# Kernel optimization log

Measured on AMD Instinct MI355X. Metric: run time of the kernel, lower is better.

The kernel has to match this reference:

```python
import jax, jax.numpy as jnp
import numpy as np

B, N, E, C_IN, C_OUT = 16, 4096, 131072, 256, 256


def setup_inputs() -> dict:
    key = jax.random.key(0)
    k1, k2, k3, k4 = jax.random.split(key, 4)
    x = jax.random.normal(k1, (B, N, C_IN), dtype=jnp.float32)
    edge_index = jax.random.randint(k2, (B, 2, E), 0, N, dtype=jnp.int32)
    edge_weight = jax.random.uniform(k3, (B, E), dtype=jnp.float32)
    # glorot init for weight [C_in, C_out]
    scale = float(np.sqrt(6.0 / (C_IN + C_OUT)))
    W = jax.random.uniform(k4, (C_IN, C_OUT), dtype=jnp.float32, minval=-scale, maxval=scale)
    return {"x": x, "edge_index": edge_index, "edge_weight": edge_weight, "W": W}


def _gcn_one_graph(xi, ei, ewi, W):
    # xi: [N, C_in], ei: [2, E+N], ewi: [E+N]
    n = xi.shape[0]
    row, col = ei[0], ei[1]
    deg = jax.ops.segment_sum(ewi, row, num_segments=n)            # [N]
    deg_inv = jnp.where(deg > 0, jax.lax.rsqrt(deg), 0.0)          # deg^-0.5, inf -> 0
    norm = deg_inv[row] * ewi * deg_inv[col]                       # [E+N]
    xw = xi @ W                                                    # [N, C_out]
    msg = norm[:, None] * xw[col]                                  # gather + scale
    out = jax.ops.segment_sum(msg, row, num_segments=n)            # scatter-add to rows
    return jax.nn.relu(out)                                        # act = F.relu, bias=False


def reference(x, edge_index, edge_weight, W):
    b, n, _ = x.shape
    # add self loops with weight 1 (fill_value=1)
    loop = jnp.arange(n, dtype=edge_index.dtype)
    loop_idx = jnp.broadcast_to(jnp.stack([loop, loop])[None], (b, 2, n))
    ei = jnp.concatenate([edge_index, loop_idx], axis=-1)          # [B, 2, E+N]
    ew = jnp.concatenate([edge_weight, jnp.ones((b, n), x.dtype)], axis=-1)  # [B, E+N]
    return jax.vmap(_gcn_one_graph, in_axes=(0, 0, 0, None))(x, ei, ew, W)
```

## Files before the change

### kernel.cpp

```cpp
#include <hip/hip_runtime.h>
#include <cstdint>
#include <cstddef>

#define BB 16
#define NN 4096
#define EE 131072
#define CIN 256
#define COUT 256
#define NCH 16
#define CHE (EE / NCH)

typedef __attribute__((ext_vector_type(8))) _Float16 h16x8;
typedef __attribute__((ext_vector_type(4))) float f32x4;

#define GLDS16(g, l) __builtin_amdgcn_global_load_lds( \
    (const __attribute__((address_space(1))) uint32_t*)(g), \
    (__attribute__((address_space(3))) uint32_t*)(l), 16, 0, 0)

__global__ __launch_bounds__(256) void phaseA_kernel(const float* __restrict__ x, _Float16* __restrict__ xh,
                                                     const float* __restrict__ W, _Float16* __restrict__ wt,
                                                     const int* __restrict__ ei, const float* __restrict__ ew,
                                                     int* __restrict__ chist, float* __restrict__ wdeg) {
    __shared__ int h[NN];
    __shared__ float wh[NN];
    int bid = blockIdx.x;
    int tid = threadIdx.x;
    if (bid < BB * NCH) {
        int b = bid >> 4, c = bid & (NCH - 1);
        for (int i = tid; i < NN; i += 256) { h[i] = 0; wh[i] = 0.f; }
        __syncthreads();
        const int* rows = ei + (size_t)b * 2 * EE + (size_t)c * CHE;
        const float* w = ew + (size_t)b * EE + (size_t)c * CHE;
        #pragma unroll 4
        for (int j = 0; j < CHE / 256; ++j) {
            int row = rows[j * 256 + tid];
            float wv = w[j * 256 + tid];
            atomicAdd(&h[row], 1);
            atomicAdd(&wh[row], wv);
        }
        __syncthreads();
        int* co = chist + ((size_t)b * NCH + c) * NN;
        float* wo = wdeg + ((size_t)b * NCH + c) * NN;
        for (int i = tid; i < NN; i += 256) { co[i] = h[i]; wo[i] = wh[i]; }
    } else if (bid < BB * NCH + (BB * NN * CIN) / (256 * 8)) {
        size_t u = (size_t)(bid - BB * NCH) * 256 + tid;
        const float* g = &x[u * 8];
        float4 f0 = *reinterpret_cast<const float4*>(g);
        float4 f1 = *reinterpret_cast<const float4*>(g + 4);
        h16x8 v;
        v[0] = (_Float16)f0.x; v[1] = (_Float16)f0.y; v[2] = (_Float16)f0.z; v[3] = (_Float16)f0.w;
        v[4] = (_Float16)f1.x; v[5] = (_Float16)f1.y; v[6] = (_Float16)f1.z; v[7] = (_Float16)f1.w;
        *reinterpret_cast<h16x8*>(&xh[u * 8]) = v;
    } else {
        int n = bid - (BB * NCH + (BB * NN * CIN) / (256 * 8));
        int k = tid;
        wt[n * CIN + k] = (_Float16)W[(size_t)k * COUT + n];
    }
}

__global__ __launch_bounds__(1024) void scanfused_kernel(const int* __restrict__ chist, const float* __restrict__ wdeg,
                                                         int* __restrict__ chunkbase, int* __restrict__ roff,
                                                         float* __restrict__ dinv) {
    int b = blockIdx.x, tid = threadIdx.x;
    int wid = tid >> 6, lane = tid & 63;
    __shared__ int wsum[16];
    __shared__ int wbase[16];
    __shared__ int gtot_s;
    int carry = 0;
    for (int g = 0; g < 4; ++g) {
        int r = g * 1024 + tid;
        int cv[NCH];
        int tot = 0;
        float dsum = 1.0f;
        #pragma unroll
        for (int c = 0; c < NCH; ++c) {
            size_t idx = ((size_t)b * NCH + c) * NN + r;
            cv[c] = chist[idx];
            tot += cv[c];
            dsum += wdeg[idx];
        }
        dinv[b * NN + r] = rsqrtf(dsum);
        int incl = tot;
        #pragma unroll
        for (int off = 1; off < 64; off <<= 1) {
            int t = __shfl_up(incl, off, 64);
            if (lane >= off) incl += t;
        }
        if (lane == 63) wsum[wid] = incl;
        __syncthreads();
        if (wid == 0) {
            int v = (lane < 16) ? wsum[lane] : 0;
            int winc = v;
            #pragma unroll
            for (int off = 1; off < 16; off <<= 1) {
                int t = __shfl_up(winc, off, 64);
                if (lane >= off) winc += t;
            }
            if (lane < 16) wbase[lane] = winc - v;
            if (lane == 15) gtot_s = winc;
        }
        __syncthreads();
        int excl = carry + wbase[wid] + (incl - tot);
        roff[b * NN + r] = excl;
        int acc = excl;
        #pragma unroll
        for (int c = 0; c < NCH; ++c) {
            chunkbase[((size_t)b * NCH + c) * NN + r] = acc;
            acc += cv[c];
        }
        carry += gtot_s;
        __syncthreads();
    }
}

__global__ __launch_bounds__(256) void gemm_glds_kernel(const _Float16* __restrict__ xh, const _Float16* __restrict__ wt,
                                                        _Float16* __restrict__ xw) {
    __shared__ _Float16 As[128 * 64];
    __shared__ _Float16 Bs[128 * 64];
    int tid = threadIdx.x;
    int lane = tid & 63;
    int wave = tid >> 6;
    int bx = blockIdx.x >> 1, by = blockIdx.x & 1;
    int row0 = bx * 128, col0 = by * 128;
    int wr = wave >> 1, wc = wave & 1;
    int hi = lane >> 4, lo = lane & 15;
    int lr = lane >> 3, lk = (lane & 7) * 8;
    f32x4 acc[4][4] = {};

    for (int kk = 0; kk < CIN; kk += 64) {
        #pragma unroll
        for (int j = 0; j < 4; ++j) {
            int seg = j * 4 + wave;
            const _Float16* ga = &xh[(size_t)(row0 + seg * 8 + lr) * CIN + kk + lk];
            const _Float16* gb = &wt [(size_t)(col0 + seg * 8 + lr) * CIN + kk + lk];
            GLDS16(ga, &As[seg * 512]);
            GLDS16(gb, &Bs[seg * 512]);
        }
        __syncthreads();
        #pragma unroll
        for (int ks = 0; ks < 2; ++ks) {
            h16x8 a[4], b[4];
            #pragma unroll
            for (int m = 0; m < 4; ++m)
                a[m] = *reinterpret_cast<const h16x8*>(&As[(wr * 64 + m * 16 + lo) * 64 + ks * 32 + 8 * hi]);
            #pragma unroll
            for (int n = 0; n < 4; ++n)
                b[n] = *reinterpret_cast<const h16x8*>(&Bs[(wc * 64 + n * 16 + lo) * 64 + ks * 32 + 8 * hi]);
            #pragma unroll
            for (int m = 0; m < 4; ++m)
                #pragma unroll
                for (int n = 0; n < 4; ++n)
                    acc[m][n] = __builtin_amdgcn_mfma_f32_16x16x32_f16(a[m], b[n], acc[m][n], 0, 0, 0);
        }
        __syncthreads();
    }
    #pragma unroll
    for (int m = 0; m < 4; ++m)
        #pragma unroll
        for (int n = 0; n < 4; ++n)
            #pragma unroll
            for (int r = 0; r < 4; ++r) {
                int row = row0 + wr * 64 + m * 16 + hi * 4 + r;
                int col = col0 + wc * 64 + n * 16 + lo;
                xw[(size_t)row * COUT + col] = (_Float16)acc[m][n][r];
            }
}

__global__ __launch_bounds__(256) void scatter2_kernel(const int* __restrict__ ei, const float* __restrict__ ew,
                                                       const float* __restrict__ dinv, const int* __restrict__ chunkbase,
                                                       int2* __restrict__ csr) {
    __shared__ int basebuf[NN];
    __shared__ float dinvs[NN];
    int bid = blockIdx.x;
    int xcd = bid & 7;
    int j = bid >> 3;
    int b = xcd * 2 + (j >> 4);
    int c = j & (NCH - 1);
    int tid = threadIdx.x;
    for (int i = tid; i < NN; i += 256) {
        basebuf[i] = chunkbase[((size_t)b * NCH + c) * NN + i];
        dinvs[i] = dinv[b * NN + i];
    }
    __syncthreads();
    const int* rows = ei + (size_t)b * 2 * EE + (size_t)c * CHE;
    const int* cols = rows + EE;
    const float* w = ew + (size_t)b * EE + (size_t)c * CHE;
    int2* cs = csr + (size_t)b * EE;
    #pragma unroll 4
    for (int jj = 0; jj < CHE / 256; ++jj) {
        int e = jj * 256 + tid;
        int row = rows[e];
        int col = cols[e];
        float nm = dinvs[row] * w[e] * dinvs[col];
        int pos = atomicAdd(&basebuf[row], 1);
        int2 pk; pk.x = col * (COUT * 2); pk.y = __float_as_int(nm);
        cs[pos] = pk;
    }
}

#define ACCH(nm, r) { \
    a0 += (nm) * (float)(r)[0]; a1 += (nm) * (float)(r)[1]; \
    a2 += (nm) * (float)(r)[2]; a3 += (nm) * (float)(r)[3]; \
    a4 += (nm) * (float)(r)[4]; a5 += (nm) * (float)(r)[5]; \
    a6 += (nm) * (float)(r)[6]; a7 += (nm) * (float)(r)[7]; }

__global__ __launch_bounds__(256) void aggregate_kernel(const _Float16* __restrict__ xw, const float* __restrict__ dinv,
                                                        const int* __restrict__ roff, const int2* __restrict__ csr,
                                                        float* __restrict__ out) {
    int bid = blockIdx.x;
    int xcd = bid & 7;
    int idx = bid >> 3;
    int b = xcd * 2 + (idx >> 10);
    int rowblk = idx & 1023;
    int wave = threadIdx.x >> 6;
    int lane = threadIdx.x & 63;
    int n = rowblk * 4 + wave;
    bool hiHalf = lane >= 32;
    int sub = lane & 31;
    int lanebyte = sub * 16;

    const int* rb = roff + b * NN;
    int s = __builtin_amdgcn_readfirstlane(rb[n]);
    int eRaw = (n == NN - 1) ? EE : rb[n + 1];
    int e = __builtin_amdgcn_readfirstlane(eRaw);
    int cnt = e - s;
    const int2* cs = csr + (size_t)b * EE + s;

    const char* xwbase = (const char*)(xw + (size_t)b * NN * COUT);
    float a0 = 0.f, a1 = 0.f, a2 = 0.f, a3 = 0.f, a4 = 0.f, a5 = 0.f, a6 = 0.f, a7 = 0.f;

    {
        float di = dinv[b * NN + n];
        float sn = hiHalf ? 0.f : di * di;
        h16x8 r = *reinterpret_cast<const h16x8*>(xwbase + (size_t)n * (COUT * 2) + lanebyte);
        ACCH(sn, r);
    }

    int m = cnt & ~7;
    int i = 0;
    for (; i < m; i += 8) {
        int2 q[8];
        #pragma unroll
        for (int u = 0; u < 8; ++u) q[u] = cs[i + u];
        #pragma unroll
        for (int u = 0; u < 4; ++u) {
            int offx = (hiHalf ? q[2 * u + 1].x : q[2 * u].x) + lanebyte;
            float nm = __int_as_float(hiHalf ? q[2 * u + 1].y : q[2 * u].y);
            h16x8 r = *reinterpret_cast<const h16x8*>(xwbase + (uint32_t)offx);
            ACCH(nm, r);
        }
    }
    if (i < cnt) {
        #pragma unroll
        for (int u = 0; u < 4; ++u) {
            int j0 = i + 2 * u, j1 = j0 + 1;
            int jc0 = (j0 < cnt) ? j0 : cnt - 1;
            int jc1 = (j1 < cnt) ? j1 : cnt - 1;
            int2 q0 = cs[jc0];
            int2 q1 = cs[jc1];
            int offx = (hiHalf ? q1.x : q0.x) + lanebyte;
            float nm0 = (j0 < cnt) ? __int_as_float(q0.y) : 0.f;
            float nm1 = (j1 < cnt) ? __int_as_float(q1.y) : 0.f;
            float nm = hiHalf ? nm1 : nm0;
            h16x8 r = *reinterpret_cast<const h16x8*>(xwbase + (uint32_t)offx);
            ACCH(nm, r);
        }
    }

    a0 += __shfl(a0, lane ^ 32, 64); a1 += __shfl(a1, lane ^ 32, 64);
    a2 += __shfl(a2, lane ^ 32, 64); a3 += __shfl(a3, lane ^ 32, 64);
    a4 += __shfl(a4, lane ^ 32, 64); a5 += __shfl(a5, lane ^ 32, 64);
    a6 += __shfl(a6, lane ^ 32, 64); a7 += __shfl(a7, lane ^ 32, 64);

    float4 o = hiHalf
        ? make_float4(fmaxf(a4, 0.f), fmaxf(a5, 0.f), fmaxf(a6, 0.f), fmaxf(a7, 0.f))
        : make_float4(fmaxf(a0, 0.f), fmaxf(a1, 0.f), fmaxf(a2, 0.f), fmaxf(a3, 0.f));
    float* orow = out + ((size_t)b * NN + n) * COUT + sub * 8 + (hiHalf ? 4 : 0);
    *reinterpret_cast<float4*>(orow) = o;
}

__global__ __launch_bounds__(256) void cvt_wt_kernel(const float* __restrict__ W, _Float16* __restrict__ wt) {
    int n = blockIdx.x;
    int k = threadIdx.x;
    wt[n * CIN + k] = (_Float16)W[(size_t)k * COUT + n];
}

__global__ __launch_bounds__(256) void init_deg_kernel(float* __restrict__ deg, float v) {
    int i = blockIdx.x * 256 + threadIdx.x;
    if (i < BB * NN) deg[i] = v;
}

__global__ __launch_bounds__(256) void deg_only_kernel(const int* __restrict__ ei, const float* __restrict__ ew,
                                                       float* __restrict__ deg) {
    int idx = blockIdx.x * 256 + threadIdx.x;
    if (idx >= BB * EE) return;
    int b = idx / EE, e = idx - b * EE;
    atomicAdd(&deg[b * NN + ei[(size_t)b * 2 * EE + e]], ew[(size_t)b * EE + e]);
}

__global__ __launch_bounds__(256) void deginv_kernel(const float* __restrict__ deg, float* __restrict__ dinv) {
    int i = blockIdx.x * 256 + threadIdx.x;
    if (i < BB * NN) {
        float d = deg[i];
        dinv[i] = (d > 0.0f) ? rsqrtf(d) : 0.0f;
    }
}

__global__ __launch_bounds__(256) void gemm_f32src_kernel(const float* __restrict__ x, const _Float16* __restrict__ wt,
                                                          _Float16* __restrict__ xw) {
    __shared__ _Float16 As[128][64];
    __shared__ _Float16 Bs[128][64];
    int tid = threadIdx.x;
    int lane = tid & 63;
    int wave = tid >> 6;
    int row0 = blockIdx.x * 128;
    int col0 = blockIdx.y * 128;
    int wr = wave >> 1, wc = wave & 1;
    int hi = lane >> 4, lo = lane & 15;
    f32x4 acc[4][4] = {};
    for (int kk = 0; kk < CIN; kk += 64) {
        #pragma unroll
        for (int j = 0; j < 4; ++j) {
            int c = j * 256 + tid;
            int r = c >> 3, kq = c & 7;
            const float* g = &x[(size_t)(row0 + r) * CIN + kk + 8 * kq];
            float4 f0 = *reinterpret_cast<const float4*>(g);
            float4 f1 = *reinterpret_cast<const float4*>(g + 4);
            h16x8 v;
            v[0] = (_Float16)f0.x; v[1] = (_Float16)f0.y; v[2] = (_Float16)f0.z; v[3] = (_Float16)f0.w;
            v[4] = (_Float16)f1.x; v[5] = (_Float16)f1.y; v[6] = (_Float16)f1.z; v[7] = (_Float16)f1.w;
            *reinterpret_cast<h16x8*>(&As[r][8 * kq]) = v;
        }
        #pragma unroll
        for (int j = 0; j < 4; ++j) {
            int c = j * 256 + tid;
            int r = c >> 3, kq = c & 7;
            *reinterpret_cast<h16x8*>(&Bs[r][8 * kq]) =
                *reinterpret_cast<const h16x8*>(&wt[(size_t)(col0 + r) * CIN + kk + 8 * kq]);
        }
        __syncthreads();
        #pragma unroll
        for (int ks = 0; ks < 2; ++ks) {
            h16x8 a[4], b[4];
            #pragma unroll
            for (int m = 0; m < 4; ++m)
                a[m] = *reinterpret_cast<const h16x8*>(&As[wr * 64 + m * 16 + lo][ks * 32 + 8 * hi]);
            #pragma unroll
            for (int n = 0; n < 4; ++n)
                b[n] = *reinterpret_cast<const h16x8*>(&Bs[wc * 64 + n * 16 + lo][ks * 32 + 8 * hi]);
            #pragma unroll
            for (int m = 0; m < 4; ++m)
                #pragma unroll
                for (int n = 0; n < 4; ++n)
                    acc[m][n] = __builtin_amdgcn_mfma_f32_16x16x32_f16(a[m], b[n], acc[m][n], 0, 0, 0);
        }
        __syncthreads();
    }
    #pragma unroll
    for (int m = 0; m < 4; ++m)
        #pragma unroll
        for (int n = 0; n < 4; ++n)
            #pragma unroll
            for (int r = 0; r < 4; ++r) {
                int row = row0 + wr * 64 + m * 16 + hi * 4 + r;
                int col = col0 + wc * 64 + n * 16 + lo;
                xw[(size_t)row * COUT + col] = (_Float16)acc[m][n][r];
            }
}

__global__ __launch_bounds__(256) void self_kernel(const _Float16* __restrict__ xw, const float* __restrict__ dinv,
                                                   float* __restrict__ out) {
    int bn = blockIdx.x;
    int c = threadIdx.x;
    float di = dinv[bn];
    out[(size_t)bn * COUT + c] = di * di * (float)xw[(size_t)bn * COUT + c];
}

__global__ __launch_bounds__(256) void scatter_atomic_kernel(const int* __restrict__ ei, const float* __restrict__ ew,
                                                             const float* __restrict__ dinv,
                                                             const _Float16* __restrict__ xw, float* __restrict__ out) {
    int be = blockIdx.x;
    int b = be / EE, e = be - b * EE;
    int c = threadIdx.x;
    int row = ei[(size_t)b * 2 * EE + e];
    int col = ei[(size_t)b * 2 * EE + EE + e];
    float w = ew[(size_t)b * EE + e];
    float nm = dinv[b * NN + row] * w * dinv[b * NN + col];
    const _Float16* xwb = xw + (size_t)b * NN * COUT;
    atomicAdd(&out[((size_t)b * NN + row) * COUT + c], nm * (float)xwb[(size_t)col * COUT + c]);
}

__global__ __launch_bounds__(256) void relu_kernel(float* __restrict__ out) {
    size_t i = (size_t)blockIdx.x * 256 + threadIdx.x;
    out[i] = fmaxf(out[i], 0.0f);
}

extern "C" void kernel_launch(void* const* d_in, const int* in_sizes, int n_in,
                              void* d_out, int out_size, void* d_ws, size_t ws_size,
                              hipStream_t stream) {
    const float* x  = (const float*)d_in[0];
    const int*   ei = (const int*)d_in[1];
    const float* ew = (const float*)d_in[2];
    const float* Wm = (const float*)d_in[3];
    float* out = (float*)d_out;

    char* ws = (char*)d_ws;
    size_t off = 0;
    auto alloc = [&](size_t bytes) -> void* {
        void* p = ws + off;
        off += (bytes + 255) & ~(size_t)255;
        return p;
    };
    _Float16* xw        = (_Float16*)alloc((size_t)BB * NN * COUT * 2);
    _Float16* xh        = (_Float16*)alloc((size_t)BB * NN * CIN * 2);
    int*      chist     = (int*)alloc((size_t)BB * NCH * NN * 4);
    float*    wdeg      = (float*)alloc((size_t)BB * NCH * NN * 4);
    int*      chunkbase = (int*)alloc((size_t)BB * NCH * NN * 4);
    int*      roff      = (int*)alloc((size_t)BB * NN * 4);
    float*    dinv      = (float*)alloc((size_t)BB * NN * 4);
    _Float16* wt        = (_Float16*)alloc((size_t)CIN * COUT * 2);
    int2*     csr       = (int2*)xh;
    float*    deg_fb    = (float*)chist;
    bool use_csr = (ws_size >= off);

    if (use_csr) {
        const int xcvtBlocks = (BB * NN * CIN) / (256 * 8);
        phaseA_kernel<<<BB * NCH + xcvtBlocks + COUT, 256, 0, stream>>>(x, xh, Wm, wt, ei, ew, chist, wdeg);
        scanfused_kernel<<<BB, 1024, 0, stream>>>(chist, wdeg, chunkbase, roff, dinv);
        gemm_glds_kernel<<<(BB * NN / 128) * (COUT / 128), 256, 0, stream>>>(xh, wt, xw);
        scatter2_kernel<<<BB * NCH, 256, 0, stream>>>(ei, ew, dinv, chunkbase, csr);
        aggregate_kernel<<<BB * NN / 4, 256, 0, stream>>>(xw, dinv, roff, csr, out);
    } else {
        const int bnBlocks = (BB * NN) / 256;
        cvt_wt_kernel<<<COUT, CIN, 0, stream>>>(Wm, wt);
        init_deg_kernel<<<bnBlocks, 256, 0, stream>>>(deg_fb, 1.0f);
        deg_only_kernel<<<(BB * EE) / 256, 256, 0, stream>>>(ei, ew, deg_fb);
        deginv_kernel<<<bnBlocks, 256, 0, stream>>>(deg_fb, dinv);
        dim3 ggrid((BB * NN) / 128, COUT / 128);
        gemm_f32src_kernel<<<ggrid, 256, 0, stream>>>(x, wt, xw);
        self_kernel<<<BB * NN, 256, 0, stream>>>(xw, dinv, out);
        scatter_atomic_kernel<<<BB * EE, 256, 0, stream>>>(ei, ew, dinv, xw, out);
        relu_kernel<<<(BB * NN * COUT) / 256, 256, 0, stream>>>(out);
    }
}
```

Before: 135.6 us.

## Fuse fp32-to-fp16 conversion of x into a full-width GEMM and use fma_mix aggregation

Drops the separate pass that converted x to fp16 in phaseA, so the GEMM now loads fp32 x directly and converts it while staging into LDS. Each GEMM block now covers all 256 output columns (128x256 tile, 8 column fragments per wave), so x is read once rather than once per column half. The aggregation inner loop replaces the half-to-float conversions plus multiply-adds with inline v_fma_mix_f32 on packed halves. The CSR buffer gets its own workspace allocation instead of aliasing xh. The trade-offs are losing the async global_load_lds staging, more accumulator registers per wave and therefore lower occupancy, and a grid half as large.

```diff
diff --git a/kernel.cpp b/kernel.cpp
--- a/kernel.cpp
+++ b/kernel.cpp
@@ -13,12 +13,7 @@
 typedef __attribute__((ext_vector_type(8))) _Float16 h16x8;
 typedef __attribute__((ext_vector_type(4))) float f32x4;
 
-#define GLDS16(g, l) __builtin_amdgcn_global_load_lds( \
-    (const __attribute__((address_space(1))) uint32_t*)(g), \
-    (__attribute__((address_space(3))) uint32_t*)(l), 16, 0, 0)
-
-__global__ __launch_bounds__(256) void phaseA_kernel(const float* __restrict__ x, _Float16* __restrict__ xh,
-                                                     const float* __restrict__ W, _Float16* __restrict__ wt,
+__global__ __launch_bounds__(256) void phaseA_kernel(const float* __restrict__ W, _Float16* __restrict__ wt,
                                                      const int* __restrict__ ei, const float* __restrict__ ew,
                                                      int* __restrict__ chist, float* __restrict__ wdeg) {
     __shared__ int h[NN];
@@ -42,17 +37,8 @@
         int* co = chist + ((size_t)b * NCH + c) * NN;
         float* wo = wdeg + ((size_t)b * NCH + c) * NN;
         for (int i = tid; i < NN; i += 256) { co[i] = h[i]; wo[i] = wh[i]; }
-    } else if (bid < BB * NCH + (BB * NN * CIN) / (256 * 8)) {
-        size_t u = (size_t)(bid - BB * NCH) * 256 + tid;
-        const float* g = &x[u * 8];
-        float4 f0 = *reinterpret_cast<const float4*>(g);
-        float4 f1 = *reinterpret_cast<const float4*>(g + 4);
-        h16x8 v;
-        v[0] = (_Float16)f0.x; v[1] = (_Float16)f0.y; v[2] = (_Float16)f0.z; v[3] = (_Float16)f0.w;
-        v[4] = (_Float16)f1.x; v[5] = (_Float16)f1.y; v[6] = (_Float16)f1.z; v[7] = (_Float16)f1.w;
-        *reinterpret_cast<h16x8*>(&xh[u * 8]) = v;
     } else {
-        int n = bid - (BB * NCH + (BB * NN * CIN) / (256 * 8));
+        int n = bid - BB * NCH;
         int k = tid;
         wt[n * CIN + k] = (_Float16)W[(size_t)k * COUT + n];
     }
@@ -113,43 +99,52 @@
     }
 }
 
-__global__ __launch_bounds__(256) void gemm_glds_kernel(const _Float16* __restrict__ xh, const _Float16* __restrict__ wt,
-                                                        _Float16* __restrict__ xw) {
+__global__ __launch_bounds__(256) void gemm_f32wide_kernel(const float* __restrict__ x, const _Float16* __restrict__ wt,
+                                                           _Float16* __restrict__ xw) {
     __shared__ _Float16 As[128 * 64];
-    __shared__ _Float16 Bs[128 * 64];
+    __shared__ _Float16 Bs[256 * 64];
     int tid = threadIdx.x;
     int lane = tid & 63;
     int wave = tid >> 6;
-    int bx = blockIdx.x >> 1, by = blockIdx.x & 1;
-    int row0 = bx * 128, col0 = by * 128;
+    int row0 = blockIdx.x * 128;
     int wr = wave >> 1, wc = wave & 1;
     int hi = lane >> 4, lo = lane & 15;
-    int lr = lane >> 3, lk = (lane & 7) * 8;
-    f32x4 acc[4][4] = {};
+    f32x4 acc[4][8] = {};
 
     for (int kk = 0; kk < CIN; kk += 64) {
         #pragma unroll
         for (int j = 0; j < 4; ++j) {
-            int seg = j * 4 + wave;
-            const _Float16* ga = &xh[(size_t)(row0 + seg * 8 + lr) * CIN + kk + lk];
-            const _Float16* gb = &wt [(size_t)(col0 + seg * 8 + lr) * CIN + kk + lk];
-            GLDS16(ga, &As[seg * 512]);
-            GLDS16(gb, &Bs[seg * 512]);
+            int c = j * 256 + tid;
+            int r = c >> 3, kq = c & 7;
+            const float* g = &x[(size_t)(row0 + r) * CIN + kk + 8 * kq];
+            float4 f0 = *reinterpret_cast<const float4*>(g);
+            float4 f1 = *reinterpret_cast<const float4*>(g + 4);
+            h16x8 v;
+            v[0] = (_Float16)f0.x; v[1] = (_Float16)f0.y; v[2] = (_Float16)f0.z; v[3] = (_Float16)f0.w;
+            v[4] = (_Float16)f1.x; v[5] = (_Float16)f1.y; v[6] = (_Float16)f1.z; v[7] = (_Float16)f1.w;
+            *reinterpret_cast<h16x8*>(&As[r * 64 + 8 * kq]) = v;
+        }
+        #pragma unroll
+        for (int j = 0; j < 8; ++j) {
+            int c = j * 256 + tid;
+            int r = c >> 3, kq = c & 7;
+            *reinterpret_cast<h16x8*>(&Bs[r * 64 + 8 * kq]) =
+                *reinterpret_cast<const h16x8*>(&wt[(size_t)r * CIN + kk + 8 * kq]);
         }
         __syncthreads();
         #pragma unroll
         for (int ks = 0; ks < 2; ++ks) {
-            h16x8 a[4], b[4];
+            h16x8 a[4], b[8];
             #pragma unroll
             for (int m = 0; m < 4; ++m)
                 a[m] = *reinterpret_cast<const h16x8*>(&As[(wr * 64 + m * 16 + lo) * 64 + ks * 32 + 8 * hi]);
             #pragma unroll
-            for (int n = 0; n < 4; ++n)
-                b[n] = *reinterpret_cast<const h16x8*>(&Bs[(wc * 64 + n * 16 + lo) * 64 + ks * 32 + 8 * hi]);
+            for (int n = 0; n < 8; ++n)
+                b[n] = *reinterpret_cast<const h16x8*>(&Bs[(wc * 128 + n * 16 + lo) * 64 + ks * 32 + 8 * hi]);
             #pragma unroll
             for (int m = 0; m < 4; ++m)
                 #pragma unroll
-                for (int n = 0; n < 4; ++n)
+                for (int n = 0; n < 8; ++n)
                     acc[m][n] = __builtin_amdgcn_mfma_f32_16x16x32_f16(a[m], b[n], acc[m][n], 0, 0, 0);
         }
         __syncthreads();
@@ -157,11 +152,11 @@
     #pragma unroll
     for (int m = 0; m < 4; ++m)
         #pragma unroll
-        for (int n = 0; n < 4; ++n)
+        for (int n = 0; n < 8; ++n)
             #pragma unroll
             for (int r = 0; r < 4; ++r) {
                 int row = row0 + wr * 64 + m * 16 + hi * 4 + r;
-                int col = col0 + wc * 64 + n * 16 + lo;
+                int col = wc * 128 + n * 16 + lo;
                 xw[(size_t)row * COUT + col] = (_Float16)acc[m][n][r];
             }
 }
@@ -198,11 +193,15 @@
     }
 }
 
-#define ACCH(nm, r) { \
-    a0 += (nm) * (float)(r)[0]; a1 += (nm) * (float)(r)[1]; \
-    a2 += (nm) * (float)(r)[2]; a3 += (nm) * (float)(r)[3]; \
-    a4 += (nm) * (float)(r)[4]; a5 += (nm) * (float)(r)[5]; \
-    a6 += (nm) * (float)(r)[6]; a7 += (nm) * (float)(r)[7]; }
+#define MIXLO(acc_, w_, nm_) asm("v_fma_mix_f32 %0, %1, %2, %0 op_sel:[0,0,0] op_sel_hi:[1,0,0]" \
+                                 : "+v"(acc_) : "v"(w_), "v"(nm_));
+#define MIXHI(acc_, w_, nm_) asm("v_fma_mix_f32 %0, %1, %2, %0 op_sel:[1,0,0] op_sel_hi:[1,0,0]" \
+                                 : "+v"(acc_) : "v"(w_), "v"(nm_));
+#define ACCMIX(w_, nm_) { \
+    MIXLO(a0, (w_).x, nm_); MIXHI(a1, (w_).x, nm_); \
+    MIXLO(a2, (w_).y, nm_); MIXHI(a3, (w_).y, nm_); \
+    MIXLO(a4, (w_).z, nm_); MIXHI(a5, (w_).z, nm_); \
+    MIXLO(a6, (w_).w, nm_); MIXHI(a7, (w_).w, nm_); }
 
 __global__ __launch_bounds__(256) void aggregate_kernel(const _Float16* __restrict__ xw, const float* __restrict__ dinv,
                                                         const int* __restrict__ roff, const int2* __restrict__ csr,
@@ -232,8 +231,8 @@
     {
         float di = dinv[b * NN + n];
         float sn = hiHalf ? 0.f : di * di;
-        h16x8 r = *reinterpret_cast<const h16x8*>(xwbase + (size_t)n * (COUT * 2) + lanebyte);
-        ACCH(sn, r);
+        uint4 w = *reinterpret_cast<const uint4*>(xwbase + (size_t)n * (COUT * 2) + lanebyte);
+        ACCMIX(w, sn);
     }
 
     int m = cnt & ~7;
@@ -246,8 +245,8 @@
         for (int u = 0; u < 4; ++u) {
             int offx = (hiHalf ? q[2 * u + 1].x : q[2 * u].x) + lanebyte;
             float nm = __int_as_float(hiHalf ? q[2 * u + 1].y : q[2 * u].y);
-            h16x8 r = *reinterpret_cast<const h16x8*>(xwbase + (uint32_t)offx);
-            ACCH(nm, r);
+            uint4 w = *reinterpret_cast<const uint4*>(xwbase + (uint32_t)offx);
+            ACCMIX(w, nm);
         }
     }
     if (i < cnt) {
@@ -262,8 +261,8 @@
             float nm0 = (j0 < cnt) ? __int_as_float(q0.y) : 0.f;
             float nm1 = (j1 < cnt) ? __int_as_float(q1.y) : 0.f;
             float nm = hiHalf ? nm1 : nm0;
-            h16x8 r = *reinterpret_cast<const h16x8*>(xwbase + (uint32_t)offx);
-            ACCH(nm, r);
+            uint4 w = *reinterpret_cast<const uint4*>(xwbase + (uint32_t)offx);
+            ACCMIX(w, nm);
         }
     }
 
@@ -412,22 +411,20 @@
         return p;
     };
     _Float16* xw        = (_Float16*)alloc((size_t)BB * NN * COUT * 2);
-    _Float16* xh        = (_Float16*)alloc((size_t)BB * NN * CIN * 2);
+    int2*     csr       = (int2*)alloc((size_t)BB * EE * 8);
     int*      chist     = (int*)alloc((size_t)BB * NCH * NN * 4);
     float*    wdeg      = (float*)alloc((size_t)BB * NCH * NN * 4);
     int*      chunkbase = (int*)alloc((size_t)BB * NCH * NN * 4);
     int*      roff      = (int*)alloc((size_t)BB * NN * 4);
     float*    dinv      = (float*)alloc((size_t)BB * NN * 4);
     _Float16* wt        = (_Float16*)alloc((size_t)CIN * COUT * 2);
-    int2*     csr       = (int2*)xh;
     float*    deg_fb    = (float*)chist;
     bool use_csr = (ws_size >= off);
 
     if (use_csr) {
-        const int xcvtBlocks = (BB * NN * CIN) / (256 * 8);
-        phaseA_kernel<<<BB * NCH + xcvtBlocks + COUT, 256, 0, stream>>>(x, xh, Wm, wt, ei, ew, chist, wdeg);
+        phaseA_kernel<<<BB * NCH + COUT, 256, 0, stream>>>(Wm, wt, ei, ew, chist, wdeg);
         scanfused_kernel<<<BB, 1024, 0, stream>>>(chist, wdeg, chunkbase, roff, dinv);
-        gemm_glds_kernel<<<(BB * NN / 128) * (COUT / 128), 256, 0, stream>>>(xh, wt, xw);
+        gemm_f32wide_kernel<<<BB * NN / 128, 256, 0, stream>>>(x, wt, xw);
         scatter2_kernel<<<BB * NCH, 256, 0, stream>>>(ei, ew, dinv, chunkbase, csr);
         aggregate_kernel<<<BB * NN / 4, 256, 0, stream>>>(xw, dinv, roff, csr, out);
     } else {
```

Result: slower. 139.9 us (+3.2%).

## Fuse CSR scatter into GEMM launch and pack CSR entries to 32 bits

Applied to the files above, without the earlier changes.

Runs the CSR scatter blocks and the fp16 GEMM tiles in a single launch so the two independent stages overlap. CSR entries are packed into one 32-bit word holding a 16-bit column and an fp16 norm, halving CSR traffic. The aggregate kernel decodes them with v_fma_mix_f32 inline asm, avoiding separate half-to-float conversions. The fp16 norm reduces precision, and the CSR buffer now reuses the degree-histogram workspace.

```diff
diff --git a/kernel.cpp b/kernel.cpp
--- a/kernel.cpp
+++ b/kernel.cpp
@@ -113,99 +113,106 @@
     }
 }
 
-__global__ __launch_bounds__(256) void gemm_glds_kernel(const _Float16* __restrict__ xh, const _Float16* __restrict__ wt,
-                                                        _Float16* __restrict__ xw) {
-    __shared__ _Float16 As[128 * 64];
-    __shared__ _Float16 Bs[128 * 64];
+__global__ __launch_bounds__(256) void gemm_scatter_kernel(const _Float16* __restrict__ xh, const _Float16* __restrict__ wt,
+                                                           _Float16* __restrict__ xw,
+                                                           const int* __restrict__ ei, const float* __restrict__ ew,
+                                                           const float* __restrict__ dinv, const int* __restrict__ chunkbase,
+                                                           uint32_t* __restrict__ csr) {
+    __shared__ __align__(16) char smem[32768];
+    int bid = blockIdx.x;
     int tid = threadIdx.x;
-    int lane = tid & 63;
-    int wave = tid >> 6;
-    int bx = blockIdx.x >> 1, by = blockIdx.x & 1;
-    int row0 = bx * 128, col0 = by * 128;
-    int wr = wave >> 1, wc = wave & 1;
-    int hi = lane >> 4, lo = lane & 15;
-    int lr = lane >> 3, lk = (lane & 7) * 8;
-    f32x4 acc[4][4] = {};
-
-    for (int kk = 0; kk < CIN; kk += 64) {
-        #pragma unroll
-        for (int j = 0; j < 4; ++j) {
-            int seg = j * 4 + wave;
-            const _Float16* ga = &xh[(size_t)(row0 + seg * 8 + lr) * CIN + kk + lk];
-            const _Float16* gb = &wt [(size_t)(col0 + seg * 8 + lr) * CIN + kk + lk];
-            GLDS16(ga, &As[seg * 512]);
-            GLDS16(gb, &Bs[seg * 512]);
-        }
-        __syncthreads();
-        #pragma unroll
-        for (int ks = 0; ks < 2; ++ks) {
-            h16x8 a[4], b[4];
-            #pragma unroll
-            for (int m = 0; m < 4; ++m)
-                a[m] = *reinterpret_cast<const h16x8*>(&As[(wr * 64 + m * 16 + lo) * 64 + ks * 32 + 8 * hi]);
-            #pragma unroll
-            for (int n = 0; n < 4; ++n)
-                b[n] = *reinterpret_cast<const h16x8*>(&Bs[(wc * 64 + n * 16 + lo) * 64 + ks * 32 + 8 * hi]);
-            #pragma unroll
-            for (int m = 0; m < 4; ++m)
+    if (bid < 256) {
+        int* basebuf = (int*)smem;
+        float* dinvs = (float*)(smem + 16384);
+        int b = bid >> 4, c = bid & (NCH - 1);
+        for (int i = tid; i < NN; i += 256) {
+            basebuf[i] = chunkbase[((size_t)b * NCH + c) * NN + i];
+            dinvs[i] = dinv[b * NN + i];
+        }
+        __syncthreads();
+        const int* rows = ei + (size_t)b * 2 * EE + (size_t)c * CHE;
+        const int* cols = rows + EE;
+        const float* w = ew + (size_t)b * EE + (size_t)c * CHE;
+        uint32_t* cs = csr + (size_t)b * EE;
+        #pragma unroll 4
+        for (int jj = 0; jj < CHE / 256; ++jj) {
+            int e = jj * 256 + tid;
+            int row = rows[e];
+            int col = cols[e];
+            float nm = dinvs[row] * w[e] * dinvs[col];
+            int pos = atomicAdd(&basebuf[row], 1);
+            uint32_t nmh = (uint32_t)__builtin_bit_cast(unsigned short, (_Float16)nm);
+            cs[pos] = ((uint32_t)col << 16) | nmh;
+        }
+    } else {
+        _Float16* As = (_Float16*)smem;
+        _Float16* Bs = As + 128 * 64;
+        int g = bid - 256;
+        int lane = tid & 63;
+        int wave = tid >> 6;
+        int bx = g >> 1, by = g & 1;
+        int row0 = bx * 128, col0 = by * 128;
+        int wr = wave >> 1, wc = wave & 1;
+        int hi = lane >> 4, lo = lane & 15;
+        int lr = lane >> 3, lk = (lane & 7) * 8;
+        f32x4 acc[4][4] = {};
+
+        for (int kk = 0; kk < CIN; kk += 64) {
+            #pragma unroll
+            for (int j = 0; j < 4; ++j) {
+                int seg = j * 4 + wave;
+                const _Float16* ga = &xh[(size_t)(row0 + seg * 8 + lr) * CIN + kk + lk];
+                const _Float16* gb = &wt [(size_t)(col0 + seg * 8 + lr) * CIN + kk + lk];
+                GLDS16(ga, &As[seg * 512]);
+                GLDS16(gb, &Bs[seg * 512]);
+            }
+            __syncthreads();
+            #pragma unroll
+            for (int ks = 0; ks < 2; ++ks) {
+                h16x8 a[4], b[4];
+                #pragma unroll
+                for (int m = 0; m < 4; ++m)
+                    a[m] = *reinterpret_cast<const h16x8*>(&As[(wr * 64 + m * 16 + lo) * 64 + ks * 32 + 8 * hi]);
                 #pragma unroll
                 for (int n = 0; n < 4; ++n)
-                    acc[m][n] = __builtin_amdgcn_mfma_f32_16x16x32_f16(a[m], b[n], acc[m][n], 0, 0, 0);
-        }
-        __syncthreads();
-    }
-    #pragma unroll
-    for (int m = 0; m < 4; ++m)
-        #pragma unroll
-        for (int n = 0; n < 4; ++n)
-            #pragma unroll
-            for (int r = 0; r < 4; ++r) {
-                int row = row0 + wr * 64 + m * 16 + hi * 4 + r;
-                int col = col0 + wc * 64 + n * 16 + lo;
-                xw[(size_t)row * COUT + col] = (_Float16)acc[m][n][r];
+                    b[n] = *reinterpret_cast<const h16x8*>(&Bs[(wc * 64 + n * 16 + lo) * 64 + ks * 32 + 8 * hi]);
+                #pragma unroll
+                for (int m = 0; m < 4; ++m)
+                    #pragma unroll
+                    for (int n = 0; n < 4; ++n)
+                        acc[m][n] = __builtin_amdgcn_mfma_f32_16x16x32_f16(a[m], b[n], acc[m][n], 0, 0, 0);
             }
-}
-
-__global__ __launch_bounds__(256) void scatter2_kernel(const int* __restrict__ ei, const float* __restrict__ ew,
-                                                       const float* __restrict__ dinv, const int* __restrict__ chunkbase,
-                                                       int2* __restrict__ csr) {
-    __shared__ int basebuf[NN];
-    __shared__ float dinvs[NN];
-    int bid = blockIdx.x;
-    int xcd = bid & 7;
-    int j = bid >> 3;
-    int b = xcd * 2 + (j >> 4);
-    int c = j & (NCH - 1);
-    int tid = threadIdx.x;
-    for (int i = tid; i < NN; i += 256) {
-        basebuf[i] = chunkbase[((size_t)b * NCH + c) * NN + i];
-        dinvs[i] = dinv[b * NN + i];
-    }
-    __syncthreads();
-    const int* rows = ei + (size_t)b * 2 * EE + (size_t)c * CHE;
-    const int* cols = rows + EE;
-    const float* w = ew + (size_t)b * EE + (size_t)c * CHE;
-    int2* cs = csr + (size_t)b * EE;
-    #pragma unroll 4
-    for (int jj = 0; jj < CHE / 256; ++jj) {
-        int e = jj * 256 + tid;
-        int row = rows[e];
-        int col = cols[e];
-        float nm = dinvs[row] * w[e] * dinvs[col];
-        int pos = atomicAdd(&basebuf[row], 1);
-        int2 pk; pk.x = col * (COUT * 2); pk.y = __float_as_int(nm);
-        cs[pos] = pk;
-    }
-}
-
-#define ACCH(nm, r) { \
-    a0 += (nm) * (float)(r)[0]; a1 += (nm) * (float)(r)[1]; \
-    a2 += (nm) * (float)(r)[2]; a3 += (nm) * (float)(r)[3]; \
-    a4 += (nm) * (float)(r)[4]; a5 += (nm) * (float)(r)[5]; \
-    a6 += (nm) * (float)(r)[6]; a7 += (nm) * (float)(r)[7]; }
+            __syncthreads();
+        }
+        #pragma unroll
+        for (int m = 0; m < 4; ++m)
+            #pragma unroll
+            for (int n = 0; n < 4; ++n)
+                #pragma unroll
+                for (int r = 0; r < 4; ++r) {
+                    int row = row0 + wr * 64 + m * 16 + hi * 4 + r;
+                    int col = col0 + wc * 64 + n * 16 + lo;
+                    xw[(size_t)row * COUT + col] = (_Float16)acc[m][n][r];
+                }
+    }
+}
+
+#define MIXQLO(acc_, w_, qv_) asm("v_fma_mix_f32 %0, %1, %2, %0 op_sel:[0,0,0] op_sel_hi:[1,1,0]" \
+                                  : "+v"(acc_) : "v"(w_), "v"(qv_));
+#define MIXQHI(acc_, w_, qv_) asm("v_fma_mix_f32 %0, %1, %2, %0 op_sel:[1,0,0] op_sel_hi:[1,1,0]" \
+                                  : "+v"(acc_) : "v"(w_), "v"(qv_));
+#define ACCMIXQ(w_, qv_) { \
+    MIXQLO(a0, (w_).x, qv_); MIXQHI(a1, (w_).x, qv_); \
+    MIXQLO(a2, (w_).y, qv_); MIXQHI(a3, (w_).y, qv_); \
+    MIXQLO(a4, (w_).z, qv_); MIXQHI(a5, (w_).z, qv_); \
+    MIXQLO(a6, (w_).w, qv_); MIXQHI(a7, (w_).w, qv_); }
+#define MIXSLO(acc_, w_, nm_) asm("v_fma_mix_f32 %0, %1, %2, %0 op_sel:[0,0,0] op_sel_hi:[1,0,0]" \
+                                  : "+v"(acc_) : "v"(w_), "v"(nm_));
+#define MIXSHI(acc_, w_, nm_) asm("v_fma_mix_f32 %0, %1, %2, %0 op_sel:[1,0,0] op_sel_hi:[1,0,0]" \
+                                  : "+v"(acc_) : "v"(w_), "v"(nm_));
 
 __global__ __launch_bounds__(256) void aggregate_kernel(const _Float16* __restrict__ xw, const float* __restrict__ dinv,
-                                                        const int* __restrict__ roff, const int2* __restrict__ csr,
+                                                        const int* __restrict__ roff, const uint32_t* __restrict__ csr,
                                                         float* __restrict__ out) {
     int bid = blockIdx.x;
     int xcd = bid & 7;
@@ -217,14 +224,14 @@
     int n = rowblk * 4 + wave;
     bool hiHalf = lane >= 32;
     int sub = lane & 31;
-    int lanebyte = sub * 16;
+    uint32_t lanebyte = sub * 16;
 
     const int* rb = roff + b * NN;
     int s = __builtin_amdgcn_readfirstlane(rb[n]);
     int eRaw = (n == NN - 1) ? EE : rb[n + 1];
     int e = __builtin_amdgcn_readfirstlane(eRaw);
     int cnt = e - s;
-    const int2* cs = csr + (size_t)b * EE + s;
+    const uint32_t* cs = csr + (size_t)b * EE + s;
 
     const char* xwbase = (const char*)(xw + (size_t)b * NN * COUT);
     float a0 = 0.f, a1 = 0.f, a2 = 0.f, a3 = 0.f, a4 = 0.f, a5 = 0.f, a6 = 0.f, a7 = 0.f;
@@ -232,38 +239,39 @@
     {
         float di = dinv[b * NN + n];
         float sn = hiHalf ? 0.f : di * di;
-        h16x8 r = *reinterpret_cast<const h16x8*>(xwbase + (size_t)n * (COUT * 2) + lanebyte);
-        ACCH(sn, r);
+        uint4 w = *reinterpret_cast<const uint4*>(xwbase + (size_t)n * (COUT * 2) + lanebyte);
+        MIXSLO(a0, w.x, sn); MIXSHI(a1, w.x, sn);
+        MIXSLO(a2, w.y, sn); MIXSHI(a3, w.y, sn);
+        MIXSLO(a4, w.z, sn); MIXSHI(a5, w.z, sn);
+        MIXSLO(a6, w.w, sn); MIXSHI(a7, w.w, sn);
     }
 
     int m = cnt & ~7;
     int i = 0;
     for (; i < m; i += 8) {
-        int2 q[8];
+        uint32_t q[8];
         #pragma unroll
         for (int u = 0; u < 8; ++u) q[u] = cs[i + u];
         #pragma unroll
         for (int u = 0; u < 4; ++u) {
-            int offx = (hiHalf ? q[2 * u + 1].x : q[2 * u].x) + lanebyte;
-            float nm = __int_as_float(hiHalf ? q[2 * u + 1].y : q[2 * u].y);
-            h16x8 r = *reinterpret_cast<const h16x8*>(xwbase + (uint32_t)offx);
-            ACCH(nm, r);
+            uint32_t qv = hiHalf ? q[2 * u + 1] : q[2 * u];
+            uint32_t offx = ((qv >> 16) << 9) + lanebyte;
+            uint4 w = *reinterpret_cast<const uint4*>(xwbase + offx);
+            ACCMIXQ(w, qv);
         }
     }
     if (i < cnt) {
         #pragma unroll
         for (int u = 0; u < 4; ++u) {
             int j0 = i + 2 * u, j1 = j0 + 1;
-            int jc0 = (j0 < cnt) ? j0 : cnt - 1;
-            int jc1 = (j1 < cnt) ? j1 : cnt - 1;
-            int2 q0 = cs[jc0];
-            int2 q1 = cs[jc1];
-            int offx = (hiHalf ? q1.x : q0.x) + lanebyte;
-            float nm0 = (j0 < cnt) ? __int_as_float(q0.y) : 0.f;
-            float nm1 = (j1 < cnt) ? __int_as_float(q1.y) : 0.f;
-            float nm = hiHalf ? nm1 : nm0;
-            h16x8 r = *reinterpret_cast<const h16x8*>(xwbase + (uint32_t)offx);
-            ACCH(nm, r);
+            uint32_t q0 = cs[(j0 < cnt) ? j0 : cnt - 1];
+            uint32_t q1 = cs[(j1 < cnt) ? j1 : cnt - 1];
+            if (j0 >= cnt) q0 &= 0xFFFF0000u;
+            if (j1 >= cnt) q1 &= 0xFFFF0000u;
+            uint32_t qv = hiHalf ? q1 : q0;
+            uint32_t offx = ((qv >> 16) << 9) + lanebyte;
+            uint4 w = *reinterpret_cast<const uint4*>(xwbase + offx);
+            ACCMIXQ(w, qv);
         }
     }
 
@@ -419,7 +427,7 @@
     int*      roff      = (int*)alloc((size_t)BB * NN * 4);
     float*    dinv      = (float*)alloc((size_t)BB * NN * 4);
     _Float16* wt        = (_Float16*)alloc((size_t)CIN * COUT * 2);
-    int2*     csr       = (int2*)xh;
+    uint32_t* csr       = (uint32_t*)chist;
     float*    deg_fb    = (float*)chist;
     bool use_csr = (ws_size >= off);
 
@@ -427,8 +435,8 @@
         const int xcvtBlocks = (BB * NN * CIN) / (256 * 8);
         phaseA_kernel<<<BB * NCH + xcvtBlocks + COUT, 256, 0, stream>>>(x, xh, Wm, wt, ei, ew, chist, wdeg);
         scanfused_kernel<<<BB, 1024, 0, stream>>>(chist, wdeg, chunkbase, roff, dinv);
-        gemm_glds_kernel<<<(BB * NN / 128) * (COUT / 128), 256, 0, stream>>>(xh, wt, xw);
-        scatter2_kernel<<<BB * NCH, 256, 0, stream>>>(ei, ew, dinv, chunkbase, csr);
+        gemm_scatter_kernel<<<256 + (BB * NN / 128) * (COUT / 128), 256, 0, stream>>>(
+            xh, wt, xw, ei, ew, dinv, chunkbase, csr);
         aggregate_kernel<<<BB * NN / 4, 256, 0, stream>>>(xw, dinv, roff, csr, out);
     } else {
         const int bnBlocks = (BB * NN) / 256;
```

Result: no change. 135.1 us (-0.4%).
